# Kernel optimization log

Hardware: AMD Instinct MI355X
Metric: run time of the kernel (lower is better)

## Reference

```python
import jax, jax.numpy as jnp
import numpy as np

# ---- config (JambaConfig defaults) ----
D_MODEL = 2048
D_STATE = 128
D_CONV = 4
EXPAND = 2
HEADDIM = 64
D_INNER = EXPAND * D_MODEL           # 4096
NHEADS = D_INNER // HEADDIM          # 64
CONV_DIM = D_INNER + 2 * D_STATE     # 4352
IN_PROJ = 2 * D_INNER + 2 * D_STATE + NHEADS  # 8512
INTER = 5632                         # ((2048*8/3)+255)//256*256
EPS = 1e-6
CHUNK = 128                          # SSD chunk length


def rmsnorm(x, w, eps=EPS):
    var = jnp.mean(jnp.square(x), axis=-1, keepdims=True)
    return x * jax.lax.rsqrt(var + eps) * w


def dw_causal_conv(x, w, b):
    # x: [B,L,C], w: [C,K] depthwise, b: [C]; causal (left pad K-1)
    xt = jnp.transpose(x, (0, 2, 1))                       # [B,C,L]
    xt = jnp.pad(xt, ((0, 0), (0, 0), (D_CONV - 1, 0)))
    y = jax.lax.conv_general_dilated(
        xt, w[:, None, :], window_strides=(1,), padding='VALID',
        feature_group_count=w.shape[0], dimension_numbers=('NCH', 'OIH', 'NCH'))
    y = y + b[None, :, None]
    return jnp.transpose(y, (0, 2, 1))                     # [B,L,C]


def segsum(x):
    # x: [..., T] -> [..., T, T] with out[l,s] = sum_{s<i<=l} x[i], -inf above diag
    T = x.shape[-1]
    xx = jnp.broadcast_to(x[..., None], (*x.shape, T))     # xx[...,i,j] = x[...,i]
    xx = jnp.where(jnp.tril(jnp.ones((T, T), bool), -1), xx, 0.0)
    s = jnp.cumsum(xx, axis=-2)
    return jnp.where(jnp.tril(jnp.ones((T, T), bool), 0), s, -jnp.inf)


def ssd(x, dt, A, Bm, Cm):
    # Mamba2 SSD (chunked selective scan). x:[b,l,h,p] dt:[b,l,h] A:[h] Bm/Cm:[b,l,n]
    b, l, h, p = x.shape
    n = Bm.shape[-1]
    c = l // CHUNK
    xr = x.reshape(b, c, CHUNK, h, p)
    dtr = dt.reshape(b, c, CHUNK, h)
    Br = Bm.reshape(b, c, CHUNK, n)
    Cr = Cm.reshape(b, c, CHUNK, n)
    dA = jnp.transpose(dtr * A, (0, 3, 1, 2))              # [b,h,c,q], all <= 0
    A_cum = jnp.cumsum(dA, axis=-1)                        # [b,h,c,q]
    L = jnp.exp(segsum(dA))                                # [b,h,c,q,q] lower-tri decays
    xdt = xr * dtr[..., None]                              # [b,c,q,h,p]
    # intra-chunk (diagonal blocks)
    Y_diag = jnp.einsum('bcln,bcsn,bhcls,bcshp->bclhp', Cr, Br, L, xdt)
    # chunk-final states
    decay_states = jnp.exp(A_cum[..., -1:] - A_cum)        # [b,h,c,q]
    states = jnp.einsum('bcln,bhcl,bclhp->bchpn', Br, decay_states, xdt)
    # inter-chunk recurrence (parallel via decay matrix over chunks)
    A_last = A_cum[..., -1]                                # [b,h,c]
    decay_chunk = jnp.exp(segsum(jnp.pad(A_last, ((0, 0), (0, 0), (1, 0)))))  # [b,h,c+1,c+1]
    states_cat = jnp.concatenate([jnp.zeros_like(states[:, :1]), states], axis=1)  # [b,c+1,h,p,n]
    new_states = jnp.einsum('bhzc,bchpn->bzhpn', decay_chunk, states_cat)
    prev = new_states[:, :-1]                              # state entering each chunk
    state_decay = jnp.exp(A_cum)                           # [b,h,c,q]
    Y_off = jnp.einsum('bcln,bchpn,bhcl->bclhp', Cr, prev, state_decay)
    return (Y_diag + Y_off).reshape(b, l, h, p)


def setup_inputs() -> dict:
    key = jax.random.key(0)
    ks = jax.random.split(key, 10)
    B, L = 2, 2048
    s = 0.02
    return {
        'hidden_states': jax.random.normal(ks[0], (B, L, D_MODEL), jnp.float32),
        'norm1_w': jnp.ones((D_MODEL,), jnp.float32),
        'in_proj_w': jax.random.normal(ks[1], (D_MODEL, IN_PROJ), jnp.float32) * s,
        'conv_w': jax.random.normal(ks[2], (CONV_DIM, D_CONV), jnp.float32) * 0.1,
        'conv_b': jnp.zeros((CONV_DIM,), jnp.float32),
        'dt_bias': jax.random.uniform(ks[3], (NHEADS,), jnp.float32, -4.0, -1.0),
        'A_log': jnp.log(jnp.arange(1, NHEADS + 1, dtype=jnp.float32)),
        'D_param': jnp.ones((NHEADS,), jnp.float32),
        'mixer_norm_w': jnp.ones((D_INNER,), jnp.float32),
        'out_proj_w': jax.random.normal(ks[4], (D_INNER, D_MODEL), jnp.float32) * s,
        'norm2_w': jnp.ones((D_MODEL,), jnp.float32),
        'gate_w': jax.random.normal(ks[5], (D_MODEL, INTER), jnp.float32) * s,
        'up_w': jax.random.normal(ks[6], (D_MODEL, INTER), jnp.float32) * s,
        'down_w': jax.random.normal(ks[7], (INTER, D_MODEL), jnp.float32) * s,
    }


def reference(hidden_states, norm1_w, in_proj_w, conv_w, conv_b, dt_bias, A_log,
              D_param, mixer_norm_w, out_proj_w, norm2_w, gate_w, up_w, down_w):
    B, L, _ = hidden_states.shape
    # --- norm1 + Mamba2 mixer + residual ---
    res = hidden_states
    h = rmsnorm(hidden_states, norm1_w)
    zxbcdt = h @ in_proj_w                                  # [B,L,8512]
    z = zxbcdt[..., :D_INNER]
    xBC = zxbcdt[..., D_INNER:D_INNER + CONV_DIM]
    dt = jax.nn.softplus(zxbcdt[..., -NHEADS:] + dt_bias)   # [B,L,H]
    xBC = jax.nn.silu(dw_causal_conv(xBC, conv_w, conv_b))
    xs = xBC[..., :D_INNER].reshape(B, L, NHEADS, HEADDIM)
    Bm = xBC[..., D_INNER:D_INNER + D_STATE]
    Cm = xBC[..., D_INNER + D_STATE:]
    A = -jnp.exp(A_log)
    y = ssd(xs, dt, A, Bm, Cm)
    y = y + D_param[None, None, :, None] * xs               # skip D term
    y = y.reshape(B, L, D_INNER)
    y = rmsnorm(y * jax.nn.silu(z), mixer_norm_w)           # gated RMSNorm
    h1 = res + y @ out_proj_w
    # --- norm2 + SwiGLU MLP + residual ---
    h2 = rmsnorm(h1, norm2_w)
    mlp = (jax.nn.silu(h2 @ gate_w) * (h2 @ up_w)) @ down_w
    return h1 + mlp
```

## Files before the change

kernel.cpp:

```cpp
#include <hip/hip_runtime.h>

#define LTOT 2048
#define BATCH 2
#define NTOK 4096
#define DMODEL 2048
#define DSTATE 128
#define NH 64
#define HD 64
#define DINNER 4096
#define CONVD 4352
#define XDTC 4416
#define INP 8512
#define INTER_ 5632
#define CHUNK_ 128
#define NCH 16
#define EPSF 1e-6f

typedef __bf16 bf16x8 __attribute__((ext_vector_type(8)));
typedef float f32x4 __attribute__((ext_vector_type(4)));
typedef unsigned short u16x4 __attribute__((ext_vector_type(4)));
typedef unsigned short u16x8 __attribute__((ext_vector_type(8)));

__device__ __forceinline__ unsigned short f2b(float f){
  unsigned int u = __builtin_bit_cast(unsigned int, f);
  u += 0x7fffu + ((u >> 16) & 1u);
  return (unsigned short)(u >> 16);
}
__device__ __forceinline__ float b2f(unsigned short h){
  return __builtin_bit_cast(float, ((unsigned int)h) << 16);
}
__device__ __forceinline__ f32x4 mfma16(bf16x8 a, bf16x8 b, f32x4 c){
  return __builtin_amdgcn_mfma_f32_16x16x32_bf16(a, b, c, 0, 0, 0);
}
typedef const __attribute__((address_space(1))) void* gas_t;
typedef __attribute__((address_space(3))) void* las_t;
__device__ __forceinline__ void gload16(const void* g, void* l){
  __builtin_amdgcn_global_load_lds((gas_t)g, (las_t)l, 16, 0, 0);
}

__global__ __launch_bounds__(256) void wconv_kernel(const float* __restrict__ W,
                                                    unsigned short* __restrict__ WT,
                                                    int K, int N)
{
  __shared__ unsigned short t[64][72];
  int n0 = blockIdx.x * 64, k0 = blockIdx.y * 64;
  int tid = threadIdx.x;
  int kl = tid >> 4, nl4 = (tid & 15) * 4;
  #pragma unroll
  for (int it = 0; it < 4; it++){
    int kk = kl + it * 16;
    float4 v = make_float4(0.f, 0.f, 0.f, 0.f);
    if (n0 < N) v = *(const float4*)&W[(size_t)(k0 + kk) * N + n0 + nl4];
    t[nl4 + 0][kk] = f2b(v.x);
    t[nl4 + 1][kk] = f2b(v.y);
    t[nl4 + 2][kk] = f2b(v.z);
    t[nl4 + 3][kk] = f2b(v.w);
  }
  __syncthreads();
  int nr = tid >> 3, k8 = (tid & 7) * 8;
  #pragma unroll
  for (int it = 0; it < 2; it++){
    int nn = nr + it * 32;
    *(u16x8*)&WT[(size_t)(n0 + nn) * K + k0 + k8] = *(const u16x8*)&t[nn][k8];
  }
}

__global__ __launch_bounds__(256) void rms_kernel(const float* __restrict__ x,
                                                  const float* __restrict__ w,
                                                  unsigned short* __restrict__ out, int width)
{
  int row = blockIdx.x, tid = threadIdx.x;
  const float* xr = x + (size_t)row * width;
  unsigned short* orow = out + (size_t)row * width;
  int nv = width >> 2;
  float ss = 0.f;
  for (int i = tid; i < nv; i += 256){
    float4 v = ((const float4*)xr)[i];
    ss += v.x*v.x + v.y*v.y + v.z*v.z + v.w*v.w;
  }
  #pragma unroll
  for (int off = 32; off > 0; off >>= 1) ss += __shfl_down(ss, off, 64);
  __shared__ float red[4];
  if ((tid & 63) == 0) red[tid >> 6] = ss;
  __syncthreads();
  float tot = red[0] + red[1] + red[2] + red[3];
  float scale = rsqrtf(tot / (float)width + EPSF);
  for (int i = tid; i < nv; i += 256){
    float4 v = ((const float4*)xr)[i];
    float4 wv = ((const float4*)w)[i];
    u16x4 o = { f2b(v.x * scale * wv.x), f2b(v.y * scale * wv.y),
                f2b(v.z * scale * wv.z), f2b(v.w * scale * wv.w) };
    ((u16x4*)orow)[i] = o;
  }
}

__global__ __launch_bounds__(256) void rms_gated_kernel(const float* __restrict__ y,
                                                        const unsigned short* __restrict__ z,
                                                        const float* __restrict__ w,
                                                        unsigned short* __restrict__ out)
{
  int row = blockIdx.x, tid = threadIdx.x;
  const float* yr = y + (size_t)row * DINNER;
  const unsigned short* zr = z + (size_t)row * DINNER;
  unsigned short* orow = out + (size_t)row * DINNER;
  float g[16];
  float ss = 0.f;
  #pragma unroll
  for (int ii = 0; ii < 4; ii++){
    int i = tid + ii * 256;
    float4 yv = ((const float4*)yr)[i];
    u16x4 zv = ((const u16x4*)zr)[i];
    #pragma unroll
    for (int e = 0; e < 4; e++){
      float zf = b2f(zv[e]);
      float yf = (&yv.x)[e];
      float gg = yf * (zf / (1.f + expf(-zf)));
      g[ii * 4 + e] = gg;
      ss += gg * gg;
    }
  }
  #pragma unroll
  for (int off = 32; off > 0; off >>= 1) ss += __shfl_down(ss, off, 64);
  __shared__ float red[4];
  if ((tid & 63) == 0) red[tid >> 6] = ss;
  __syncthreads();
  float tot = red[0] + red[1] + red[2] + red[3];
  float scale = rsqrtf(tot / (float)DINNER + EPSF);
  #pragma unroll
  for (int ii = 0; ii < 4; ii++){
    int i = tid + ii * 256;
    float4 wv = ((const float4*)w)[i];
    u16x4 o;
    #pragma unroll
    for (int e = 0; e < 4; e++) o[e] = f2b(g[ii * 4 + e] * scale * (&wv.x)[e]);
    ((u16x4*)orow)[i] = o;
  }
}

__global__ __launch_bounds__(512, 2) void gemm3_kernel(const unsigned short* __restrict__ A,
                                                       const unsigned short* __restrict__ BT,
                                                       const float* __restrict__ addsrc,
                                                       float* __restrict__ Cf,
                                                       unsigned short* __restrict__ Cb,
                                                       unsigned short* __restrict__ Cb2, int splitN,
                                                       const unsigned short* __restrict__ gate,
                                                       float* __restrict__ dtraw,
                                                       int M, int N, int K)
{
  extern __shared__ unsigned short lds[];
  int tid = threadIdx.x, lane = tid & 63, w = tid >> 6;
  int wm = w >> 2, wn = w & 3;
  int bid = blockIdx.x + blockIdx.y * gridDim.x;
  int nwg = gridDim.x * gridDim.y;
  int q8 = nwg >> 3, r8 = nwg & 7;
  int xcd = bid & 7, boff = bid >> 3;
  int wgid = (xcd < r8 ? xcd * (q8 + 1) : r8 * (q8 + 1) + (xcd - r8) * q8) + boff;
  int bn = (wgid % gridDim.x) * 256;
  int bm = (wgid / gridDim.x) * 128;

  int soct8 = ((lane & 3) ^ ((lane >> 2) & 3)) << 3;
  int prow_l = (lane >> 2);
  int ko = (((lane >> 4) ^ (lane & 3)) << 3);
  int rsel = (lane & 15) * 32 + ko;

  f32x4 acc[4][4] = {};
  int NT = K >> 5;

  #define STAGE(kt, bsel)                                                              \
    {                                                                                  \
      unsigned short* bb_ = &lds[(bsel) * 12288];                                      \
      size_t k0_ = (size_t)(kt) << 5;                                                  \
      gload16(&A [(size_t)(bm +       w * 16 + prow_l) * K + k0_ + soct8], &bb_[w * 512]);            \
      gload16(&BT[(size_t)(bn +       w * 16 + prow_l) * K + k0_ + soct8], &bb_[4096 + w * 512]);     \
      gload16(&BT[(size_t)(bn + 128 + w * 16 + prow_l) * K + k0_ + soct8], &bb_[8192 + w * 512]);     \
    }

  STAGE(0, 0)
  STAGE(1, 1)
  asm volatile("s_waitcnt vmcnt(3)" ::: "memory");
  __builtin_amdgcn_s_barrier();
  asm volatile("" ::: "memory");

  for (int t = 0; t < NT; ++t){
    const unsigned short* bufc = &lds[(t % 3) * 12288];
    bf16x8 afr[4], bfr[4];
    #pragma unroll
    for (int i = 0; i < 4; ++i)
      afr[i] = *(const bf16x8*)&bufc[(wm * 64 + i * 16) * 32 + rsel];
    #pragma unroll
    for (int c = 0; c < 4; ++c)
      bfr[c] = *(const bf16x8*)&bufc[4096 + (wn * 64 + c * 16) * 32 + rsel];
    if (t + 2 < NT) STAGE(t + 2, (t + 2) % 3)
    asm volatile("s_waitcnt lgkmcnt(0)" ::: "memory");
    __builtin_amdgcn_s_setprio(1);
    #pragma unroll
    for (int i = 0; i < 4; ++i)
      #pragma unroll
      for (int c = 0; c < 4; ++c)
        acc[i][c] = mfma16(afr[i], bfr[c], acc[i][c]);
    __builtin_amdgcn_s_setprio(0);
    if (t + 2 < NT)      asm volatile("s_waitcnt vmcnt(3)" ::: "memory");
    else if (t + 1 < NT) asm volatile("s_waitcnt vmcnt(0)" ::: "memory");
    asm volatile("" ::: "memory");
    __builtin_amdgcn_s_barrier();
    asm volatile("" ::: "memory");
  }
  #undef STAGE

  int r0 = bm + wm * 64 + ((lane >> 4) << 2);
  int c0 = bn + wn * 64 + (lane & 15);
  #pragma unroll
  for (int i = 0; i < 4; ++i){
    #pragma unroll
    for (int j = 0; j < 4; ++j){
      int cc = c0 + j * 16;
      if (cc < N){
        #pragma unroll
        for (int e = 0; e < 4; ++e){
          int rr = r0 + i * 16 + e;
          float v = acc[i][j][e];
          if (Cf){
            size_t idx = (size_t)rr * N + cc;
            if (addsrc) v += addsrc[idx];
            Cf[idx] = v;
          } else if (cc < splitN){
            size_t idx = (size_t)rr * splitN + cc;
            float vv = v;
            if (gate){ float gg = b2f(gate[idx]); vv = gg / (1.f + expf(-gg)) * v; }
            Cb[idx] = f2b(vv);
          } else {
            Cb2[(size_t)rr * (N - splitN) + (cc - splitN)] = f2b(v);
            if (dtraw && cc >= N - NH) dtraw[(size_t)rr * NH + (cc - (N - NH))] = v;
          }
        }
      }
    }
  }
}

__global__ __launch_bounds__(256, 3) void gemm4_kernel(const unsigned short* __restrict__ A,
                                                       const unsigned short* __restrict__ BT,
                                                       const float* __restrict__ addsrc,
                                                       float* __restrict__ Cf,
                                                       int M, int N, int K)
{
  extern __shared__ unsigned short lds[];
  int tid = threadIdx.x, lane = tid & 63, w = tid >> 6;
  int wm = w >> 1, wn = w & 1;
  int bid = blockIdx.x + blockIdx.y * gridDim.x;
  int nwg = gridDim.x * gridDim.y;
  int q8 = nwg >> 3, r8 = nwg & 7;
  int xcd = bid & 7, boff = bid >> 3;
  int wgid = (xcd < r8 ? xcd * (q8 + 1) : r8 * (q8 + 1) + (xcd - r8) * q8) + boff;
  int bn = (wgid % gridDim.x) * 128;
  int bm = (wgid / gridDim.x) * 128;

  int soct8 = ((lane & 3) ^ ((lane >> 2) & 3)) << 3;
  int prow_l = (lane >> 2);
  int ko = (((lane >> 4) ^ (lane & 3)) << 3);
  int rsel = (lane & 15) * 32 + ko;

  f32x4 acc[4][4] = {};
  int NT = K >> 5;

  #define STAGE4(kt, bsel)                                                             \
    {                                                                                  \
      unsigned short* bb_ = &lds[(bsel) * 8192];                                       \
      size_t k0_ = (size_t)(kt) << 5;                                                  \
      gload16(&A [(size_t)(bm +      w * 16 + prow_l) * K + k0_ + soct8], &bb_[w * 512]);          \
      gload16(&A [(size_t)(bm + 64 + w * 16 + prow_l) * K + k0_ + soct8], &bb_[2048 + w * 512]);   \
      gload16(&BT[(size_t)(bn +      w * 16 + prow_l) * K + k0_ + soct8], &bb_[4096 + w * 512]);   \
      gload16(&BT[(size_t)(bn + 64 + w * 16 + prow_l) * K + k0_ + soct8], &bb_[6144 + w * 512]);   \
    }

  STAGE4(0, 0)
  STAGE4(1, 1)
  asm volatile("s_waitcnt vmcnt(4)" ::: "memory");
  __builtin_amdgcn_s_barrier();
  asm volatile("" ::: "memory");

  for (int t = 0; t < NT; ++t){
    const unsigned short* bufc = &lds[(t % 3) * 8192];
    bf16x8 afr[4], bfr[4];
    #pragma unroll
    for (int i = 0; i < 4; ++i)
      afr[i] = *(const bf16x8*)&bufc[(wm * 64 + i * 16) * 32 + rsel];
    #pragma unroll
    for (int c = 0; c < 4; ++c)
      bfr[c] = *(const bf16x8*)&bufc[4096 + (wn * 64 + c * 16) * 32 + rsel];
    if (t + 2 < NT) STAGE4(t + 2, (t + 2) % 3)
    asm volatile("s_waitcnt lgkmcnt(0)" ::: "memory");
    __builtin_amdgcn_s_setprio(1);
    #pragma unroll
    for (int i = 0; i < 4; ++i)
      #pragma unroll
      for (int c = 0; c < 4; ++c)
        acc[i][c] = mfma16(afr[i], bfr[c], acc[i][c]);
    __builtin_amdgcn_s_setprio(0);
    if (t + 2 < NT)      asm volatile("s_waitcnt vmcnt(4)" ::: "memory");
    else if (t + 1 < NT) asm volatile("s_waitcnt vmcnt(0)" ::: "memory");
    asm volatile("" ::: "memory");
    __builtin_amdgcn_s_barrier();
    asm volatile("" ::: "memory");
  }
  #undef STAGE4

  int r0 = bm + wm * 64 + ((lane >> 4) << 2);
  int c0 = bn + wn * 64 + (lane & 15);
  #pragma unroll
  for (int i = 0; i < 4; ++i){
    #pragma unroll
    for (int j = 0; j < 4; ++j){
      int cc = c0 + j * 16;
      #pragma unroll
      for (int e = 0; e < 4; ++e){
        int rr = r0 + i * 16 + e;
        size_t idx = (size_t)rr * N + cc;
        float v = acc[i][j][e];
        if (addsrc) v += addsrc[idx];
        Cf[idx] = v;
      }
    }
  }
}

__global__ __launch_bounds__(256) void dt_kernel(const float* __restrict__ dtraw,
                                                 const float* __restrict__ dt_bias,
                                                 float* __restrict__ dtb)
{
  int idx = blockIdx.x * 256 + threadIdx.x;
  float raw = dtraw[idx] + dt_bias[idx & 63];
  dtb[idx] = (raw > 20.f) ? raw : log1pf(expf(raw));
}

__global__ __launch_bounds__(64) void acum_kernel(const float* __restrict__ dtb,
                                                  const float* __restrict__ A_log,
                                                  float* __restrict__ acum)
{
  int bid = blockIdx.x;
  int c = bid & 15;
  int hh = (bid >> 4) & 63;
  int b = bid >> 10;
  int lane = threadIdx.x;
  float Av = -expf(A_log[hh]);
  int rowbase = b * LTOT + c * CHUNK_;
  float v0 = dtb[(size_t)(rowbase + 2 * lane) * NH + hh] * Av;
  float v1 = dtb[(size_t)(rowbase + 2 * lane + 1) * NH + hh] * Av;
  float s = v0 + v1;
  #pragma unroll
  for (int d = 1; d < 64; d <<= 1){
    float t = __shfl_up(s, d, 64);
    if (lane >= d) s += t;
  }
  float excl = s - (v0 + v1);
  float* dst = acum + ((size_t)(b * NH + hh)) * LTOT + c * CHUNK_;
  dst[2 * lane]     = excl + v0;
  dst[2 * lane + 1] = excl + v0 + v1;
}

__global__ __launch_bounds__(256) void conv_kernel(const unsigned short* __restrict__ xdt,
                                                   const float* __restrict__ cw,
                                                   const float* __restrict__ cb,
                                                   unsigned short* __restrict__ xbc)
{
  int ch = blockIdx.x * 256 + threadIdx.x;
  int l0 = blockIdx.y * 4, b = blockIdx.z;
  float x[7];
  #pragma unroll
  for (int j = 0; j < 7; j++){
    int ls = l0 - 3 + j;
    x[j] = (ls >= 0) ? b2f(xdt[((size_t)(b * LTOT + ls)) * XDTC + ch]) : 0.f;
  }
  float w0 = cw[ch * 4 + 0], w1 = cw[ch * 4 + 1], w2 = cw[ch * 4 + 2], w3 = cw[ch * 4 + 3];
  float bias = cb[ch];
  #pragma unroll
  for (int i = 0; i < 4; i++){
    float acc = bias + x[i] * w0 + x[i + 1] * w1 + x[i + 2] * w2 + x[i + 3] * w3;
    acc = acc / (1.f + expf(-acc));
    xbc[((size_t)(b * LTOT + l0 + i)) * CONVD + ch] = f2b(acc);
  }
}

__global__ __launch_bounds__(256) void ssd_sy_kernel(const unsigned short* __restrict__ xbc,
                                                     const float* __restrict__ dtb,
                                                     const float* __restrict__ acum,
                                                     float* __restrict__ y)
{
  int hh = blockIdx.x;
  int c = blockIdx.y >> 1;
  int half = blockIdx.y & 1;
  int b = blockIdx.z;
  __shared__ unsigned short Cs[64][136];
  __shared__ unsigned short Bs[128][136];
  __shared__ float ac[128];
  int tid = threadIdx.x, lane = tid & 63, w = tid >> 6;
  int l0 = half * 64;
  size_t rowbase = (size_t)b * LTOT + c * CHUNK_;
  if (tid < 128) ac[tid] = acum[((size_t)(b * NH + hh)) * LTOT + c * CHUNK_ + tid];
  #pragma unroll
  for (int p = 0; p < 8; p++){
    int lr = p * 8 + (tid >> 5);
    int n4 = (tid & 31) * 4;
    *(u16x4*)&Cs[lr][n4] =
      *(const u16x4*)&xbc[(rowbase + l0 + lr) * CONVD + DINNER + DSTATE + n4];
  }
  #pragma unroll
  for (int p = 0; p < 16; p++){
    int s = p * 8 + (tid >> 5);
    int n4 = (tid & 31) * 4;
    *(u16x4*)&Bs[s][n4] = *(const u16x4*)&xbc[(rowbase + s) * CONVD + DINNER + n4];
  }
  __syncthreads();
  f32x4 accS[8] = {};
  #pragma unroll
  for (int kk = 0; kk < 4; kk++){
    bf16x8 a = *(const bf16x8*)&Cs[w * 16 + (lane & 15)][kk * 32 + (lane >> 4) * 8];
    #pragma unroll
    for (int fc = 0; fc < 8; fc++){
      bf16x8 bb = *(const bf16x8*)&Bs[fc * 16 + (lane & 15)][kk * 32 + (lane >> 4) * 8];
      accS[fc] = mfma16(a, bb, accS[fc]);
    }
  }
  __syncthreads();
  {
    int lr = w * 16 + ((lane >> 4) << 2);
    #pragma unroll
    for (int fc = 0; fc < 8; fc++){
      int s = fc * 16 + (lane & 15);
      #pragma unroll
      for (int j = 0; j < 4; j++){
        int l = l0 + lr + j;
        float v = (s <= l) ? accS[fc][j] * expf(ac[l] - ac[s]) : 0.f;
        Cs[lr + j][s] = f2b(v);
      }
    }
  }
  #pragma unroll
  for (int p = 0; p < 8; p++){
    int lr = p * 16 + (tid >> 4);
    int p4 = (tid & 15) * 4;
    float dtl = dtb[(rowbase + lr) * NH + hh];
    u16x4 v = *(const u16x4*)&xbc[(rowbase + lr) * CONVD + hh * HD + p4];
    Bs[p4 + 0][lr] = f2b(b2f(v[0]) * dtl);
    Bs[p4 + 1][lr] = f2b(b2f(v[1]) * dtl);
    Bs[p4 + 2][lr] = f2b(b2f(v[2]) * dtl);
    Bs[p4 + 3][lr] = f2b(b2f(v[3]) * dtl);
  }
  __syncthreads();
  f32x4 accY[4] = {};
  #pragma unroll
  for (int kk = 0; kk < 4; kk++){
    bf16x8 a = *(const bf16x8*)&Cs[w * 16 + (lane & 15)][kk * 32 + (lane >> 4) * 8];
    #pragma unroll
    for (int fc = 0; fc < 4; fc++){
      bf16x8 bb = *(const bf16x8*)&Bs[fc * 16 + (lane & 15)][kk * 32 + (lane >> 4) * 8];
      accY[fc] = mfma16(a, bb, accY[fc]);
    }
  }
  {
    int lr = w * 16 + ((lane >> 4) << 2);
    #pragma unroll
    for (int fc = 0; fc < 4; fc++){
      int p = fc * 16 + (lane & 15);
      #pragma unroll
      for (int j = 0; j < 4; j++){
        y[(rowbase + l0 + lr + j) * DINNER + hh * HD + p] = accY[fc][j];
      }
    }
  }
}

__global__ __launch_bounds__(256) void ssd_states_kernel(const unsigned short* __restrict__ xbc,
                                                         const float* __restrict__ dtb,
                                                         const float* __restrict__ acum,
                                                         unsigned short* __restrict__ states)
{
  int hh = blockIdx.x, c = blockIdx.y, b = blockIdx.z;
  __shared__ unsigned short BsT[128][136];
  __shared__ unsigned short XT[64][136];
  __shared__ float ac[128];
  int tid = threadIdx.x, lane = tid & 63, w = tid >> 6;
  size_t rowbase = (size_t)b * LTOT + c * CHUNK_;
  if (tid < 128) ac[tid] = acum[((size_t)(b * NH + hh)) * LTOT + c * CHUNK_ + tid];
  #pragma unroll
  for (int p = 0; p < 16; p++){
    int l = p * 8 + (tid >> 5);
    int n4 = (tid & 31) * 4;
    u16x4 v = *(const u16x4*)&xbc[(rowbase + l) * CONVD + DINNER + n4];
    BsT[n4 + 0][l] = v[0];
    BsT[n4 + 1][l] = v[1];
    BsT[n4 + 2][l] = v[2];
    BsT[n4 + 3][l] = v[3];
  }
  #pragma unroll
  for (int p = 0; p < 8; p++){
    int l = p * 16 + (tid >> 4);
    int p4 = (tid & 15) * 4;
    float dtl = dtb[(rowbase + l) * NH + hh];
    u16x4 v = *(const u16x4*)&xbc[(rowbase + l) * CONVD + hh * HD + p4];
    XT[p4 + 0][l] = f2b(b2f(v[0]) * dtl);
    XT[p4 + 1][l] = f2b(b2f(v[1]) * dtl);
    XT[p4 + 2][l] = f2b(b2f(v[2]) * dtl);
    XT[p4 + 3][l] = f2b(b2f(v[3]) * dtl);
  }
  __syncthreads();
  float aclast = ac[127];
  f32x4 accP[8] = {};
  #pragma unroll
  for (int kk = 0; kk < 4; kk++){
    int kbase = kk * 32 + (lane >> 4) * 8;
    union { u16x4 q[2]; unsigned short u[8]; bf16x8 v; } rw, ot;
    rw.q[0] = *(const u16x4*)&XT[w * 16 + (lane & 15)][kbase];
    rw.q[1] = *(const u16x4*)&XT[w * 16 + (lane & 15)][kbase + 4];
    #pragma unroll
    for (int e = 0; e < 8; e++){
      ot.u[e] = f2b(b2f(rw.u[e]) * expf(aclast - ac[kbase + e]));
    }
    #pragma unroll
    for (int fc = 0; fc < 8; fc++){
      bf16x8 bb = *(const bf16x8*)&BsT[fc * 16 + (lane & 15)][kbase];
      accP[fc] = mfma16(ot.v, bb, accP[fc]);
    }
  }
  size_t sbase = ((size_t)((b * NCH + c) * NH + hh)) * HD * DSTATE;
  int p0 = w * 16 + ((lane >> 4) << 2);
  #pragma unroll
  for (int fc = 0; fc < 8; fc++){
    int n = fc * 16 + (lane & 15);
    #pragma unroll
    for (int j = 0; j < 4; j++){
      states[sbase + (size_t)(p0 + j) * DSTATE + n] = f2b(accP[fc][j]);
    }
  }
}

__global__ __launch_bounds__(256) void scan_kernel(unsigned short* __restrict__ states,
                                                   const float* __restrict__ acum)
{
  int bh = blockIdx.x;
  int b = bh >> 6, hh = bh & 63;
  int jg = blockIdx.y * 4;
  int t = threadIdx.x;
  float run[4] = {0.f, 0.f, 0.f, 0.f};
  for (int c = 0; c < NCH; c++){
    float alast = acum[(size_t)bh * LTOT + c * CHUNK_ + 127];
    float dec = expf(alast);
    size_t base = ((size_t)((b * NCH + c) * NH + hh)) * (HD * DSTATE);
    #pragma unroll
    for (int j = 0; j < 4; j++){
      size_t idx = base + (size_t)(jg + j) * 256 + t;
      float sc = b2f(states[idx]);
      states[idx] = f2b(run[j]);
      run[j] = run[j] * dec + sc;
    }
  }
}

__global__ __launch_bounds__(256) void ssd3_kernel(const unsigned short* __restrict__ xbc,
                                                   const unsigned short* __restrict__ states,
                                                   const float* __restrict__ acum,
                                                   const float* __restrict__ Dp,
                                                   float* __restrict__ y)
{
  int hh = blockIdx.x, c = blockIdx.y, b = blockIdx.z;
  __shared__ unsigned short Cs[128][136];
  __shared__ unsigned short Ps[64][136];
  __shared__ float ac[128];
  int tid = threadIdx.x, lane = tid & 63, w = tid >> 6;
  size_t rowbase = (size_t)b * LTOT + c * CHUNK_;
  if (tid < 128) ac[tid] = acum[((size_t)(b * NH + hh)) * LTOT + c * CHUNK_ + tid];
  #pragma unroll
  for (int p = 0; p < 16; p++){
    int l = p * 8 + (tid >> 5);
    int n4 = (tid & 31) * 4;
    *(u16x4*)&Cs[l][n4] =
      *(const u16x4*)&xbc[(rowbase + l) * CONVD + DINNER + DSTATE + n4];
  }
  size_t sbase = ((size_t)((b * NCH + c) * NH + hh)) * (HD * DSTATE);
  #pragma unroll
  for (int p = 0; p < 8; p++){
    int pp = p * 8 + (tid >> 5);
    int n4 = (tid & 31) * 4;
    *(u16x4*)&Ps[pp][n4] = *(const u16x4*)&states[sbase + (size_t)pp * DSTATE + n4];
  }
  __syncthreads();
  f32x4 acc[2][4] = {};
  #pragma unroll
  for (int kk = 0; kk < 4; kk++){
    bf16x8 a0 = *(const bf16x8*)&Cs[w * 32 + (lane & 15)][kk * 32 + (lane >> 4) * 8];
    bf16x8 a1 = *(const bf16x8*)&Cs[w * 32 + 16 + (lane & 15)][kk * 32 + (lane >> 4) * 8];
    #pragma unroll
    for (int fc = 0; fc < 4; fc++){
      bf16x8 bb = *(const bf16x8*)&Ps[fc * 16 + (lane & 15)][kk * 32 + (lane >> 4) * 8];
      acc[0][fc] = mfma16(a0, bb, acc[0][fc]);
      acc[1][fc] = mfma16(a1, bb, acc[1][fc]);
    }
  }
  float dpar = Dp[hh];
  #pragma unroll
  for (int fr = 0; fr < 2; fr++){
    int lr = w * 32 + fr * 16 + ((lane >> 4) << 2);
    #pragma unroll
    for (int fc = 0; fc < 4; fc++){
      int p = fc * 16 + (lane & 15);
      #pragma unroll
      for (int j = 0; j < 4; j++){
        int l = lr + j;
        size_t yi = (rowbase + l) * DINNER + hh * HD + p;
        float xsv = b2f(xbc[(rowbase + l) * CONVD + hh * HD + p]);
        y[yi] += acc[fr][fc][j] * expf(ac[l]) + dpar * xsv;
      }
    }
  }
}

extern "C" void kernel_launch(void* const* d_in, const int* in_sizes, int n_in,
                              void* d_out, int out_size, void* d_ws, size_t ws_size,
                              hipStream_t stream)
{
  (void)in_sizes; (void)n_in; (void)out_size; (void)ws_size;
  const float* hidden    = (const float*)d_in[0];
  const float* norm1_w   = (const float*)d_in[1];
  const float* in_proj_w = (const float*)d_in[2];
  const float* conv_w    = (const float*)d_in[3];
  const float* conv_b    = (const float*)d_in[4];
  const float* dt_bias   = (const float*)d_in[5];
  const float* A_log     = (const float*)d_in[6];
  const float* D_param   = (const float*)d_in[7];
  const float* mixer_w   = (const float*)d_in[8];
  const float* out_proj_w= (const float*)d_in[9];
  const float* norm2_w   = (const float*)d_in[10];
  const float* gate_w    = (const float*)d_in[11];
  const float* up_w      = (const float*)d_in[12];
  const float* down_w    = (const float*)d_in[13];

  char* ws = (char*)d_ws;
  unsigned short* zbuf    = (unsigned short*)(ws);
  unsigned short* WT_gate = (unsigned short*)(ws);
  unsigned short* xdt     = (unsigned short*)(ws + 33554432ull);
  unsigned short* states  = (unsigned short*)(ws + 33554432ull);
  unsigned short* ygn     = (unsigned short*)(ws + 33554432ull);
  unsigned short* WT_up   = (unsigned short*)(ws + 33554432ull);
  unsigned short* xbc     = (unsigned short*)(ws + 69730304ull);
  unsigned short* WT_out  = (unsigned short*)(ws + 69730304ull);
  unsigned short* h2      = (unsigned short*)(ws + 69730304ull);
  unsigned short* WT_down = (unsigned short*)(ws + 69730304ull);
  float* dtraw            = (float*)(ws + 105381888ull);
  float* dtb              = (float*)(ws + 106430464ull);
  float* acum             = (float*)(ws + 107479040ull);
  float* ybuf             = (float*)(ws + 108527616ull);
  unsigned short* hbuf    = (unsigned short*)(ws + 108527616ull);
  unsigned short* gbuf    = (unsigned short*)(ws + 108527616ull);
  unsigned short* WT_in   = (unsigned short*)(ws + 125304832ull);
  float* h1               = (float*)d_out;
  float* outp             = (float*)d_out;

  const int dynLDS3 = 73728;
  const int dynLDS4 = 49152;
  hipFuncSetAttribute((const void*)gemm3_kernel,
                      hipFuncAttributeMaxDynamicSharedMemorySize, dynLDS3);
  hipFuncSetAttribute((const void*)gemm4_kernel,
                      hipFuncAttributeMaxDynamicSharedMemorySize, dynLDS4);

  wconv_kernel<<<dim3(136, 32), 256, 0, stream>>>(in_proj_w, WT_in, DMODEL, INP);
  rms_kernel<<<NTOK, 256, 0, stream>>>(hidden, norm1_w, hbuf, DMODEL);
  gemm3_kernel<<<dim3(34, 32), 512, dynLDS3, stream>>>(hbuf, WT_in, nullptr, nullptr,
                                                       zbuf, xdt, DINNER, nullptr, dtraw,
                                                       NTOK, INP, DMODEL);
  dt_kernel<<<NTOK * NH / 256, 256, 0, stream>>>(dtraw, dt_bias, dtb);
  acum_kernel<<<BATCH * NH * NCH, 64, 0, stream>>>(dtb, A_log, acum);
  conv_kernel<<<dim3(CONVD / 256, LTOT / 4, BATCH), 256, 0, stream>>>(xdt, conv_w, conv_b, xbc);
  ssd_sy_kernel<<<dim3(NH, NCH * 2, BATCH), 256, 0, stream>>>(xbc, dtb, acum, ybuf);
  ssd_states_kernel<<<dim3(NH, NCH, BATCH), 256, 0, stream>>>(xbc, dtb, acum, states);
  scan_kernel<<<dim3(BATCH * NH, 8), 256, 0, stream>>>(states, acum);
  ssd3_kernel<<<dim3(NH, NCH, BATCH), 256, 0, stream>>>(xbc, states, acum, D_param, ybuf);
  rms_gated_kernel<<<NTOK, 256, 0, stream>>>(ybuf, zbuf, mixer_w, ygn);
  wconv_kernel<<<dim3(32, 64), 256, 0, stream>>>(out_proj_w, WT_out, DINNER, DMODEL);
  gemm4_kernel<<<dim3(16, 32), 256, dynLDS4, stream>>>(ygn, WT_out, hidden, h1,
                                                       NTOK, DMODEL, DINNER);
  rms_kernel<<<NTOK, 256, 0, stream>>>(h1, norm2_w, h2, DMODEL);
  wconv_kernel<<<dim3(88, 32), 256, 0, stream>>>(gate_w, WT_gate, DMODEL, INTER_);
  gemm3_kernel<<<dim3(22, 32), 512, dynLDS3, stream>>>(h2, WT_gate, nullptr, nullptr,
                                                       gbuf, nullptr, INTER_, nullptr, nullptr,
                                                       NTOK, INTER_, DMODEL);
  wconv_kernel<<<dim3(88, 32), 256, 0, stream>>>(up_w, WT_up, DMODEL, INTER_);
  gemm3_kernel<<<dim3(22, 32), 512, dynLDS3, stream>>>(h2, WT_up, nullptr, nullptr,
                                                       gbuf, nullptr, INTER_, gbuf, nullptr,
                                                       NTOK, INTER_, DMODEL);
  wconv_kernel<<<dim3(32, 88), 256, 0, stream>>>(down_w, WT_down, INTER_, DMODEL);
  gemm4_kernel<<<dim3(16, 32), 256, dynLDS4, stream>>>(gbuf, WT_down, h1, outp,
                                                       NTOK, DMODEL, INTER_);
}
```

Before: 1.036 ms.

## Merge gate and up projections into one GEMM and drop LDS waitcnt

Concatenates the transposed gate and up weights so a single wider GEMM launch writes both outputs through the split-N path, then applies SiLU(gate)*up in a separate elementwise kernel. This is meant to fill the GPU better with one 44x32 grid instead of two 22x32 launches, at the cost of an extra pass over the intermediate activations. It also removes the explicit lgkmcnt(0) wait before the MFMA loop in both GEMM kernels and leaves LDS fragment waits to the compiler, which risks reordering hazards if the compiler does not insert them. Workspace buffers are rearranged to hold the concatenated weights and the separate up output.

```diff
diff --git a/kernel.cpp b/kernel.cpp
--- a/kernel.cpp
+++ b/kernel.cpp
@@ -137,6 +137,23 @@
   }
 }
 
+__global__ __launch_bounds__(256) void act_kernel(unsigned short* __restrict__ g,
+                                                  const unsigned short* __restrict__ u, int n8)
+{
+  int stride = gridDim.x * 256;
+  for (int i = blockIdx.x * 256 + threadIdx.x; i < n8; i += stride){
+    u16x8 gv = ((const u16x8*)g)[i];
+    u16x8 uv = ((const u16x8*)u)[i];
+    u16x8 o;
+    #pragma unroll
+    for (int e = 0; e < 8; e++){
+      float gf = b2f(gv[e]);
+      o[e] = f2b(gf / (1.f + expf(-gf)) * b2f(uv[e]));
+    }
+    ((u16x8*)g)[i] = o;
+  }
+}
+
 __global__ __launch_bounds__(512, 2) void gemm3_kernel(const unsigned short* __restrict__ A,
                                                        const unsigned short* __restrict__ BT,
                                                        const float* __restrict__ addsrc,
@@ -191,7 +208,6 @@
     for (int c = 0; c < 4; ++c)
       bfr[c] = *(const bf16x8*)&bufc[4096 + (wn * 64 + c * 16) * 32 + rsel];
     if (t + 2 < NT) STAGE(t + 2, (t + 2) % 3)
-    asm volatile("s_waitcnt lgkmcnt(0)" ::: "memory");
     __builtin_amdgcn_s_setprio(1);
     #pragma unroll
     for (int i = 0; i < 4; ++i)
@@ -289,7 +305,6 @@
     for (int c = 0; c < 4; ++c)
       bfr[c] = *(const bf16x8*)&bufc[4096 + (wn * 64 + c * 16) * 32 + rsel];
     if (t + 2 < NT) STAGE4(t + 2, (t + 2) % 3)
-    asm volatile("s_waitcnt lgkmcnt(0)" ::: "memory");
     __builtin_amdgcn_s_setprio(1);
     #pragma unroll
     for (int i = 0; i < 4; ++i)
@@ -636,15 +651,14 @@
 
   char* ws = (char*)d_ws;
   unsigned short* zbuf    = (unsigned short*)(ws);
-  unsigned short* WT_gate = (unsigned short*)(ws);
+  unsigned short* WT_cat  = (unsigned short*)(ws);
+  unsigned short* WT_down = (unsigned short*)(ws);
   unsigned short* xdt     = (unsigned short*)(ws + 33554432ull);
   unsigned short* states  = (unsigned short*)(ws + 33554432ull);
   unsigned short* ygn     = (unsigned short*)(ws + 33554432ull);
-  unsigned short* WT_up   = (unsigned short*)(ws + 33554432ull);
+  unsigned short* ubuf    = (unsigned short*)(ws + 46137344ull);
   unsigned short* xbc     = (unsigned short*)(ws + 69730304ull);
   unsigned short* WT_out  = (unsigned short*)(ws + 69730304ull);
-  unsigned short* h2      = (unsigned short*)(ws + 69730304ull);
-  unsigned short* WT_down = (unsigned short*)(ws + 69730304ull);
   float* dtraw            = (float*)(ws + 105381888ull);
   float* dtb              = (float*)(ws + 106430464ull);
   float* acum             = (float*)(ws + 107479040ull);
@@ -652,6 +666,7 @@
   unsigned short* hbuf    = (unsigned short*)(ws + 108527616ull);
   unsigned short* gbuf    = (unsigned short*)(ws + 108527616ull);
   unsigned short* WT_in   = (unsigned short*)(ws + 125304832ull);
+  unsigned short* h2      = (unsigned short*)(ws + 154664960ull);
   float* h1               = (float*)d_out;
   float* outp             = (float*)d_out;
 
@@ -679,14 +694,12 @@
   gemm4_kernel<<<dim3(16, 32), 256, dynLDS4, stream>>>(ygn, WT_out, hidden, h1,
                                                        NTOK, DMODEL, DINNER);
   rms_kernel<<<NTOK, 256, 0, stream>>>(h1, norm2_w, h2, DMODEL);
-  wconv_kernel<<<dim3(88, 32), 256, 0, stream>>>(gate_w, WT_gate, DMODEL, INTER_);
-  gemm3_kernel<<<dim3(22, 32), 512, dynLDS3, stream>>>(h2, WT_gate, nullptr, nullptr,
-                                                       gbuf, nullptr, INTER_, nullptr, nullptr,
-                                                       NTOK, INTER_, DMODEL);
-  wconv_kernel<<<dim3(88, 32), 256, 0, stream>>>(up_w, WT_up, DMODEL, INTER_);
-  gemm3_kernel<<<dim3(22, 32), 512, dynLDS3, stream>>>(h2, WT_up, nullptr, nullptr,
-                                                       gbuf, nullptr, INTER_, gbuf, nullptr,
-                                                       NTOK, INTER_, DMODEL);
+  wconv_kernel<<<dim3(88, 32), 256, 0, stream>>>(gate_w, WT_cat, DMODEL, INTER_);
+  wconv_kernel<<<dim3(88, 32), 256, 0, stream>>>(up_w, WT_cat + 11534336ull, DMODEL, INTER_);
+  gemm3_kernel<<<dim3(44, 32), 512, dynLDS3, stream>>>(h2, WT_cat, nullptr, nullptr,
+                                                       gbuf, ubuf, INTER_, nullptr, nullptr,
+                                                       NTOK, 2 * INTER_, DMODEL);
+  act_kernel<<<2048, 256, 0, stream>>>(gbuf, ubuf, NTOK * INTER_ / 8);
   wconv_kernel<<<dim3(32, 88), 256, 0, stream>>>(down_w, WT_down, INTER_, DMODEL);
   gemm4_kernel<<<dim3(16, 32), 256, dynLDS4, stream>>>(gbuf, WT_down, h1, outp,
                                                        NTOK, DMODEL, INTER_);
```

Result: faster. 1.012 ms (-2.4%).
